# Performance work log

Measured on AMD Instinct MI355X. Metric: run time of the kernel, lower is better.

Reference implementation:

```python
import jax, jax.numpy as jnp
import numpy as np

B, D, NR, H = 8, 64, 6, 3        # batch, input_dim, num_relation, num_hop
R2 = 2 * NR                      # relations incl. inverses
NUM_RULE = R2 ** H               # 1728 combinatorial rules
EPS = 1e-6
TAU = 1.0


def _rule_indices():
    # torch.meshgrid (indexing='ij') over num_hop copies of arange(2*NR), stacked on last dim
    a = np.arange(R2)
    grids = np.meshgrid(*([a] * H), indexing="ij")
    return jnp.asarray(np.stack(grids, -1).reshape(-1, H))  # [NUM_RULE, H] int


def setup_inputs() -> dict:
    key = jax.random.key(0)
    ks = jax.random.split(key, 11)
    s = 0.1
    return {
        "query": jax.random.normal(ks[0], (B, D), jnp.float32),
        "relation_emb": jax.random.normal(ks[1], (R2, D), jnp.float32) * s,      # nn.Embedding(2*NR, D)
        "indicator": jax.random.normal(ks[2], (D,), jnp.float32) * s,            # nn.Embedding(1, D)
        "rel_W": jax.random.normal(ks[3], (H, D, R2 * D), jnp.float32) * s,      # per-layer relation_linear
        "rel_b": jax.random.normal(ks[4], (H, R2 * D), jnp.float32) * s,
        "lin_W": jax.random.normal(ks[5], (H, 13 * D, D), jnp.float32) * s,      # per-layer combine Linear(13D->D)
        "lin_b": jax.random.normal(ks[6], (H, D), jnp.float32) * s,
        "mlp_W1": jax.random.normal(ks[7], (2 * D, D), jnp.float32) * s,
        "mlp_b1": jax.random.normal(ks[8], (D,), jnp.float32) * s,
        "mlp_W2": jax.random.normal(ks[9], (D, 1), jnp.float32) * s,
        "mlp_b2": jax.random.normal(ks[10], (1,), jnp.float32) * s,
    }


def reference(query, relation_emb, indicator, rel_W, rel_b, lin_W, lin_b,
              mlp_W1, mlp_b1, mlp_W2, mlp_b2):
    rel_idx = _rule_indices()                       # [R, H]
    Rn = rel_idx.shape[0]

    # PNA degree scales: each graph is a chain; degree_out+1 (boundary self-message)
    # node 0 -> 1 message (boundary only), nodes 1..H -> 2 messages (edge + boundary)
    log_deg_head = jnp.log(jnp.float32(1.0))
    log_deg_tail = jnp.log(jnp.float32(2.0))
    mean_scale = (log_deg_head + H * log_deg_tail) / (H + 1)
    s_head = log_deg_head / mean_scale
    s_tail = log_deg_tail / mean_scale
    scales_head = jnp.stack([jnp.float32(1.0), s_head, 1.0 / jnp.maximum(s_head, 1e-2)])
    scales_tail = jnp.stack([jnp.float32(1.0), s_tail, 1.0 / jnp.maximum(s_tail, 1e-2)])

    # node-0 PNA update: single message == boundary == indicator (constant across graphs)
    # stats layout per feature dim: (mean, max, min, std)
    f0 = jnp.stack([indicator, indicator, indicator,
                    jnp.full((D,), float(np.sqrt(EPS)), indicator.dtype)], -1).reshape(4 * D)
    upd0 = (f0[:, None] * scales_head).reshape(12 * D)

    # boundary / initial hidden: indicator at node 0 of every graph
    hidden = jnp.zeros((B, Rn, H + 1, D), query.dtype)
    hidden = hidden.at[:, :, 0, :].set(indicator)

    for l in range(H):
        # dependent relation table from the query (relation_linear)
        rel_table = (query @ rel_W[l] + rel_b[l]).reshape(B, R2, D)
        rel = rel_table[:, rel_idx]                 # [B, R, H, D] gather per edge
        msg = hidden[:, :, :-1, :] * rel            # distmult message on edges h -> h+1
        # tail-node PNA stats over message set {msg, boundary=0}
        mean = msg * 0.5
        mx = jnp.maximum(msg, 0.0)
        mn = jnp.minimum(msg, 0.0)
        std = jnp.sqrt(jnp.maximum(msg * msg * 0.25, EPS))   # sq_mean - mean^2 = msg^2/4
        feats = jnp.stack([mean, mx, mn, std], -1).reshape(B, Rn, H, 4 * D)
        upd_tail = (feats[..., None] * scales_tail).reshape(B, Rn, H, 12 * D)
        upd = jnp.concatenate(
            [jnp.broadcast_to(upd0, (B, Rn, 1, 12 * D)), upd_tail], axis=2)
        # combine: relu(Linear(cat([input, update])))
        hidden = jax.nn.relu(
            jnp.concatenate([hidden, upd], -1) @ lin_W[l] + lin_b[l])

    # readout at tail node H, concat per-node query
    feat = jnp.concatenate(
        [hidden[:, :, H, :], jnp.broadcast_to(query[:, None, :], (B, Rn, D))], -1)
    score = (jax.nn.relu(feat @ mlp_W1 + mlp_b1) @ mlp_W2 + mlp_b2)[..., 0]   # [B, R]
    attention = jax.nn.softmax(score / TAU, axis=-1)
    r_emb = relation_emb[rel_idx]                   # [R, H, D]
    subgoals = jnp.einsum("br,rhd->bhd", attention, r_emb)
    masks = jnp.ones((B, H), bool)
    return subgoals, masks
```

## Files before the change

kernel.cpp:

```cpp
#include <hip/hip_runtime.h>
#include <hip/hip_bf16.h>


typedef const float* fp;

#define WS_WT     0
#define WS_RELT   49152
#define WS_QW1    67584
#define WS_Q2     68096
#define WS_QW3    141824
#define WS_SCORES 142592

__device__ __forceinline__ void accq(float4 mv, float4 tv,
                                     float4 wa, float4 wb, float4 wc, float4 wd,
                                     float& acc){
  acc += mv.x*wa.x; acc += fabsf(mv.x)*wa.y; acc += tv.x*wa.z;
  acc += mv.y*wb.x; acc += fabsf(mv.y)*wb.y; acc += tv.y*wb.z;
  acc += mv.z*wc.x; acc += fabsf(mv.z)*wc.y; acc += tv.z*wc.z;
  acc += mv.w*wd.x; acc += fabsf(mv.w)*wd.y; acc += tv.w*wd.z;
}

__global__ __launch_bounds__(256) void k_pre1(fp lin_W, fp query, fp rel_W,
                       fp rel_b, fp mlp_W1, fp mlp_b1, float* ws){
  __shared__ float sW[3072];
  __shared__ float part[4][64];
  int bi = blockIdx.x, tid = threadIdx.x;

  if (bi < 48){
    int l = bi>>4, d0 = (bi&15)*4;
    fp src = lin_W + (size_t)l*832*64 + (size_t)(64 + 12*d0)*64;
    float4* s4 = (float4*)sW;
    const float4* g4 = (const float4*)src;
    s4[tid] = g4[tid]; s4[tid+256] = g4[tid+256]; s4[tid+512] = g4[tid+512];
    __syncthreads();
    int c = tid&3, j = tid>>2;
    #pragma unroll
    for (int dd=0; dd<4; dd++){
      const float* W = sW + dd*768 + j;
      float v = 0.f;
      if (c == 0){
        float w0 = W[0]   + (4.f/3.f)*W[64]  + 0.75f*W[128];
        float w1 = W[192] + (4.f/3.f)*W[256] + 0.75f*W[320];
        float w2 = W[384] + (4.f/3.f)*W[448] + 0.75f*W[512];
        v = 0.5f*w0 + 0.5f*(w1 + w2);
      } else if (c == 1){
        float w1 = W[192] + (4.f/3.f)*W[256] + 0.75f*W[320];
        float w2 = W[384] + (4.f/3.f)*W[448] + 0.75f*W[512];
        v = 0.5f*(w1 - w2);
      } else if (c == 2){
        v = 0.5f*(W[576] + (4.f/3.f)*W[640] + 0.75f*W[704]);
      }
      ws[WS_WT + l*16384 + (d0+dd)*256 + tid] = v;
    }
  } else if (bi < 336){
    int idx = bi - 48;
    int l = idx/96; int rem = idx%96; int b = rem/12; int jj = rem%12;
    int d = tid&63, kc = tid>>6;
    fp W = rel_W + (size_t)l*64*768 + (size_t)(kc*16)*768 + jj*64 + d;
    fp q = query + b*64 + kc*16;
    float acc = (kc == 0) ? rel_b[l*768 + jj*64 + d] : 0.f;
    #pragma unroll
    for (int k=0;k<16;k++) acc += q[k] * W[k*768];
    part[kc][d] = acc;
    __syncthreads();
    if (tid < 64){
      float v = ((part[0][tid] + part[1][tid]) + part[2][tid]) + part[3][tid];
      ws[WS_RELT + l*6144 + b*768 + jj*64 + tid] = v;
    }
  } else {
    int b = bi - 336;
    int j = tid&63, kc = tid>>6;
    float acc = (kc == 0) ? mlp_b1[j] : 0.f;
    fp q = query + b*64 + kc*16;
    #pragma unroll
    for (int i=0;i<16;i++) acc += q[i] * mlp_W1[(64 + kc*16 + i)*64 + j];
    part[kc][j] = acc;
    __syncthreads();
    if (tid < 64){
      float v = ((part[0][tid] + part[1][tid]) + part[2][tid]) + part[3][tid];
      ws[WS_QW1 + b*64 + tid] = v;
    }
  }
}

__global__ void k_mid(fp indicator, fp lin_W, fp lin_b, float* ws){
  __shared__ float sC2[64], sC2W[64], sP1[64], sQ3[12][64];
  __shared__ __align__(16) float mP[64], tP[64];
  __shared__ __align__(16) float mL[12][64], tL[12][64];
  int tid = threadIdx.x;
  int w = tid>>6, j = tid&63;
  bool isQ2 = blockIdx.x < 96;
  int b  = isQ2 ? blockIdx.x/12 : blockIdx.x-96;
  int i0 = isQ2 ? blockIdx.x%12 : 0;
  if (w == 0){
    float acc = lin_b[j];
    #pragma unroll 8
    for (int d=0; d<64; d++) acc += 2e-3f * ws[WS_WT + ((d<<6)+j)*4 + 2];
    sC2[j] = fmaxf(acc, 0.f);
  } else if (w == 1 && isQ2){
    const float* rel = ws + WS_RELT + (b*12+i0)*64;
    float m = indicator[j] * rel[j];
    mP[j] = m; tP[j] = fmaxf(fabsf(m), 2e-3f);
  }
  __syncthreads();
  if (w == 0){
    float a2 = lin_b[64+j];
    fp W1 = lin_W + 832*64;
    #pragma unroll 16
    for (int k=0;k<64;k++) a2 += sC2[k] * W1[k*64+j];
    sC2W[j] = a2;
  } else if (w == 1 && isQ2){
    const float4* W4 = (const float4*)(ws + WS_WT);
    float acc = lin_b[j];
    #pragma unroll
    for (int dq=0; dq<16; dq++){
      float4 mv = ((const float4*)mP)[dq], tv = ((const float4*)tP)[dq];
      float4 wa = W4[(dq*4+0)*64+j], wb = W4[(dq*4+1)*64+j],
             wc = W4[(dq*4+2)*64+j], wd = W4[(dq*4+3)*64+j];
      accq(mv,tv,wa,wb,wc,wd,acc);
    }
    sP1[j] = fmaxf(acc, 0.f);
  }
  __syncthreads();
  {
    const float* rel = ws + WS_RELT + 6144 + (b*12+w)*64;
    float s = isQ2 ? sP1[j] : sC2[j];
    float m = s * rel[j];
    mL[w][j] = m; tL[w][j] = fmaxf(fabsf(m), 2e-3f);
  }
  __syncthreads();
  const float4* W4 = (const float4*)(ws + WS_WT + 16384);
  float acc = sC2W[j];
  #pragma unroll
  for (int dq=0; dq<16; dq++){
    float4 mv = ((const float4*)mL[w])[dq], tv = ((const float4*)tL[w])[dq];
    float4 wa = W4[(dq*4+0)*64+j], wb = W4[(dq*4+1)*64+j],
           wc = W4[(dq*4+2)*64+j], wd = W4[(dq*4+3)*64+j];
    accq(mv,tv,wa,wb,wc,wd,acc);
  }
  if (isQ2){
    ws[WS_Q2 + ((b*12+i0)*12+w)*64 + j] = fmaxf(acc, 0.f);
  } else {
    sQ3[w][j] = fmaxf(acc, 0.f);
    __syncthreads();
    fp W2 = lin_W + 2*832*64;
    float a = lin_b[128+j];
    #pragma unroll 16
    for (int k=0;k<64;k++) a += sQ3[w][k]*W2[k*64+j];
    ws[WS_QW3 + (b*12+w)*64 + j] = a;
  }
}

__global__ __launch_bounds__(256) void k_score(fp mlp_W1, fp mlp_W2, float* ws){
  __shared__ float wt_s[4096];
  __shared__ float fin[4][4][64];
  __shared__ __align__(16) float m_s[4][4][64];
  __shared__ __align__(16) float t_s[4][4][64];
  int tid = threadIdx.x, w = tid>>6, j = tid&63;
  int wave = blockIdx.x*4 + w;
  int b = blockIdx.x/108;
  int rem = wave%432;
  int i0 = rem/36; int t36 = rem%36;
  int i2 = t36/3;  int i1b = (t36%3)*4;
  {
    float rl = ws[WS_RELT + 12288 + (b*12+i2)*64 + j];
    #pragma unroll
    for (int r=0;r<4;r++){
      float qv = ws[WS_Q2 + ((b*12+i0)*12 + i1b + r)*64 + j];
      float m = qv*rl;
      m_s[w][r][j] = m;
      t_s[w][r][j] = fmaxf(fabsf(m), 2e-3f);
    }
  }
  float a0 = ws[WS_QW3 + (b*12+i2)*64 + j];
  float acc[4] = {a0, a0, a0, a0};
  const float4* Wt2 = (const float4*)(ws + WS_WT + 32768);
  for (int ch=0; ch<4; ch++){
    __syncthreads();
    {
      const float4* src = Wt2 + ch*1024;
      float4* dst = (float4*)wt_s;
      #pragma unroll
      for (int k=0; k<4; k++) dst[tid + k*256] = src[tid + k*256];
    }
    __syncthreads();
    #pragma unroll
    for (int dq=0; dq<4; dq++){
      int dc = ch*4 + dq;
      const float4* wl = (const float4*)wt_s + dq*256 + j;
      float4 wa = wl[0], wb = wl[64], wc = wl[128], wd = wl[192];
      #pragma unroll
      for (int r=0;r<4;r++){
        float4 mv = ((const float4*)m_s[w][r])[dc];
        float4 tv = ((const float4*)t_s[w][r])[dc];
        accq(mv,tv,wa,wb,wc,wd,acc[r]);
      }
    }
  }
  __syncthreads();
  fin[w][0][j]=fmaxf(acc[0],0.f); fin[w][1][j]=fmaxf(acc[1],0.f);
  fin[w][2][j]=fmaxf(acc[2],0.f); fin[w][3][j]=fmaxf(acc[3],0.f);
  __syncthreads();
  float qw = ws[WS_QW1 + b*64 + j];
  float w2v = mlp_W2[j];
  float h0=qw, h1=qw, h2=qw, h3=qw;
  #pragma unroll 8
  for (int i=0;i<64;i++){
    float wv = mlp_W1[i*64+j];
    h0 += fin[w][0][i]*wv; h1 += fin[w][1][i]*wv;
    h2 += fin[w][2][i]*wv; h3 += fin[w][3][i]*wv;
  }
  float s0=fmaxf(h0,0.f)*w2v, s1=fmaxf(h1,0.f)*w2v;
  float s2=fmaxf(h2,0.f)*w2v, s3=fmaxf(h3,0.f)*w2v;
  #pragma unroll
  for (int off=32; off>0; off>>=1){
    s0 += __shfl_down(s0, off, 64); s1 += __shfl_down(s1, off, 64);
    s2 += __shfl_down(s2, off, 64); s3 += __shfl_down(s3, off, 64);
  }
  if (j == 0){
    int rbase = i0*144 + i1b*12 + i2;
    float* S = ws + WS_SCORES + b*1728 + rbase;
    S[0] = s0; S[12] = s1; S[24] = s2; S[36] = s3;
  }
}

__global__ void k_final(fp relation_emb, float* ws, float* out){
  int b = blockIdx.x, tid = threadIdx.x;
  int w = tid>>6, lane = tid&63;
  __shared__ float se[1728];
  __shared__ float wred[4];
  __shared__ float pb[36][4];
  __shared__ float bins[36];
  const float* sc = ws + WS_SCORES + b*1728;
  float mx = -1e30f;
  for (int r=tid; r<1728; r+=256){ float v = sc[r]; se[r] = v; mx = fmaxf(mx, v); }
  #pragma unroll
  for (int off=32; off>0; off>>=1) mx = fmaxf(mx, __shfl_xor(mx, off, 64));
  if (lane == 0) wred[w] = mx;
  __syncthreads();
  mx = fmaxf(fmaxf(wred[0],wred[1]), fmaxf(wred[2],wred[3]));
  __syncthreads();
  float ts = 0.f;
  for (int r=tid; r<1728; r+=256){ float e = __expf(se[r]-mx); se[r] = e; ts += e; }
  #pragma unroll
  for (int off=32; off>0; off>>=1) ts += __shfl_xor(ts, off, 64);
  if (lane == 0) wred[w] = ts;
  __syncthreads();
  float tot = (wred[0]+wred[1]) + (wred[2]+wred[3]);
  if (tid < 144){
    int bin = tid>>2, q = tid&3;
    int h = bin/12, jj = bin%12;
    float a = 0.f;
    if (h == 0){
      const float* p = se + jj*144 + q*36;
      #pragma unroll 4
      for (int k=0;k<36;k++) a += p[k];
    } else if (h == 1){
      for (int t=q*36; t<q*36+36; t++) a += se[(t/12)*144 + jj*12 + (t%12)];
    } else {
      for (int t=q*36; t<q*36+36; t++) a += se[(t/12)*144 + (t%12)*12 + jj];
    }
    pb[bin][q] = a;
  }
  __syncthreads();
  if (tid < 36) bins[tid] = (pb[tid][0]+pb[tid][1]) + (pb[tid][2]+pb[tid][3]);
  __syncthreads();
  if (tid < 192){
    int h = tid>>6, d = tid&63;
    float acc = 0.f;
    #pragma unroll
    for (int jj=0; jj<12; jj++) acc += bins[h*12+jj] * relation_emb[jj*64+d];
    out[b*192 + tid] = acc/tot;
  }
  if (tid >= 192 && tid < 195){
    out[1536 + b*3 + (tid-192)] = 1.0f;
  }
}

extern "C" void kernel_launch(void* const* d_in, const int* in_sizes, int n_in,
                              void* d_out, int out_size, void* d_ws, size_t ws_size,
                              hipStream_t stream){
  fp query        = (fp)d_in[0];
  fp relation_emb = (fp)d_in[1];
  fp indicator    = (fp)d_in[2];
  fp rel_W        = (fp)d_in[3];
  fp rel_b        = (fp)d_in[4];
  fp lin_W        = (fp)d_in[5];
  fp lin_b        = (fp)d_in[6];
  fp mlp_W1       = (fp)d_in[7];
  fp mlp_b1       = (fp)d_in[8];
  fp mlp_W2       = (fp)d_in[9];
  float* ws = (float*)d_ws;
  float* out = (float*)d_out;

  k_pre1 <<<344, 256, 0, stream>>>(lin_W, query, rel_W, rel_b, mlp_W1, mlp_b1, ws);
  k_mid  <<<104, 768, 0, stream>>>(indicator, lin_W, lin_b, ws);
  k_score<<<864, 256, 0, stream>>>(mlp_W1, mlp_W2, ws);
  k_final<<<8,   256, 0, stream>>>(relation_emb, ws, out);
}
```

Before: 114.7 us.

## Move layer-2 precompute into k_mid and recompute clamped abs in-register

Work that only layer 2 and the readout need (layer-2 weight folding, layer-2 relation projection, query MLP term) moves out of k_pre1 into extra blocks of k_mid, so it runs alongside the mid-stage compute and k_pre1 gets shorter. Separately, the stored clamped-abs array t is dropped and fmaxf(fabsf(m), 2e-3) is recomputed inside accq. This cuts shared-memory footprint and LDS reads in k_score in exchange for a few extra ALU ops per element. The idle threads in the 768-thread helper blocks waste some occupancy.

```diff
diff --git a/kernel.cpp b/kernel.cpp
--- a/kernel.cpp
+++ b/kernel.cpp
@@ -11,22 +11,22 @@
 #define WS_QW3    141824
 #define WS_SCORES 142592
 
-__device__ __forceinline__ void accq(float4 mv, float4 tv,
+__device__ __forceinline__ void accq(float4 mv,
                                      float4 wa, float4 wb, float4 wc, float4 wd,
                                      float& acc){
-  acc += mv.x*wa.x; acc += fabsf(mv.x)*wa.y; acc += tv.x*wa.z;
-  acc += mv.y*wb.x; acc += fabsf(mv.y)*wb.y; acc += tv.y*wb.z;
-  acc += mv.z*wc.x; acc += fabsf(mv.z)*wc.y; acc += tv.z*wc.z;
-  acc += mv.w*wd.x; acc += fabsf(mv.w)*wd.y; acc += tv.w*wd.z;
+  acc += mv.x*wa.x; acc += fabsf(mv.x)*wa.y; acc += fmaxf(fabsf(mv.x),2e-3f)*wa.z;
+  acc += mv.y*wb.x; acc += fabsf(mv.y)*wb.y; acc += fmaxf(fabsf(mv.y),2e-3f)*wb.z;
+  acc += mv.z*wc.x; acc += fabsf(mv.z)*wc.y; acc += fmaxf(fabsf(mv.z),2e-3f)*wc.z;
+  acc += mv.w*wd.x; acc += fabsf(mv.w)*wd.y; acc += fmaxf(fabsf(mv.w),2e-3f)*wd.z;
 }
 
 __global__ __launch_bounds__(256) void k_pre1(fp lin_W, fp query, fp rel_W,
-                       fp rel_b, fp mlp_W1, fp mlp_b1, float* ws){
+                       fp rel_b, float* ws){
   __shared__ float sW[3072];
   __shared__ float part[4][64];
   int bi = blockIdx.x, tid = threadIdx.x;
 
-  if (bi < 48){
+  if (bi < 32){
     int l = bi>>4, d0 = (bi&15)*4;
     fp src = lin_W + (size_t)l*832*64 + (size_t)(64 + 12*d0)*64;
     float4* s4 = (float4*)sW;
@@ -52,8 +52,8 @@
       }
       ws[WS_WT + l*16384 + (d0+dd)*256 + tid] = v;
     }
-  } else if (bi < 336){
-    int idx = bi - 48;
+  } else {
+    int idx = bi - 32;
     int l = idx/96; int rem = idx%96; int b = rem/12; int jj = rem%12;
     int d = tid&63, kc = tid>>6;
     fp W = rel_W + (size_t)l*64*768 + (size_t)(kc*16)*768 + jj*64 + d;
@@ -67,31 +67,89 @@
       float v = ((part[0][tid] + part[1][tid]) + part[2][tid]) + part[3][tid];
       ws[WS_RELT + l*6144 + b*768 + jj*64 + tid] = v;
     }
-  } else {
-    int b = bi - 336;
-    int j = tid&63, kc = tid>>6;
-    float acc = (kc == 0) ? mlp_b1[j] : 0.f;
-    fp q = query + b*64 + kc*16;
-    #pragma unroll
-    for (int i=0;i<16;i++) acc += q[i] * mlp_W1[(64 + kc*16 + i)*64 + j];
-    part[kc][j] = acc;
-    __syncthreads();
-    if (tid < 64){
-      float v = ((part[0][tid] + part[1][tid]) + part[2][tid]) + part[3][tid];
-      ws[WS_QW1 + b*64 + tid] = v;
-    }
-  }
-}
-
-__global__ void k_mid(fp indicator, fp lin_W, fp lin_b, float* ws){
+  }
+}
+
+__global__ __launch_bounds__(768) void k_mid(fp indicator, fp lin_W, fp lin_b,
+                       fp query, fp rel_W, fp rel_b, fp mlp_W1, fp mlp_b1,
+                       float* ws){
   __shared__ float sC2[64], sC2W[64], sP1[64], sQ3[12][64];
-  __shared__ __align__(16) float mP[64], tP[64];
-  __shared__ __align__(16) float mL[12][64], tL[12][64];
-  int tid = threadIdx.x;
+  __shared__ __align__(16) float mP[64];
+  __shared__ __align__(16) float mL[12][64];
+  __shared__ float sW[3072];
+  __shared__ float part[4][64];
+  int bi = blockIdx.x, tid = threadIdx.x;
+
+  if (bi >= 104){
+    if (bi < 120){
+      int d0 = (bi-104)*4;
+      if (tid < 256){
+        fp src = lin_W + (size_t)2*832*64 + (size_t)(64 + 12*d0)*64;
+        float4* s4 = (float4*)sW;
+        const float4* g4 = (const float4*)src;
+        s4[tid] = g4[tid]; s4[tid+256] = g4[tid+256]; s4[tid+512] = g4[tid+512];
+      }
+      __syncthreads();
+      if (tid < 256){
+        int c = tid&3, j = tid>>2;
+        #pragma unroll
+        for (int dd=0; dd<4; dd++){
+          const float* W = sW + dd*768 + j;
+          float v = 0.f;
+          if (c == 0){
+            float w0 = W[0]   + (4.f/3.f)*W[64]  + 0.75f*W[128];
+            float w1 = W[192] + (4.f/3.f)*W[256] + 0.75f*W[320];
+            float w2 = W[384] + (4.f/3.f)*W[448] + 0.75f*W[512];
+            v = 0.5f*w0 + 0.5f*(w1 + w2);
+          } else if (c == 1){
+            float w1 = W[192] + (4.f/3.f)*W[256] + 0.75f*W[320];
+            float w2 = W[384] + (4.f/3.f)*W[448] + 0.75f*W[512];
+            v = 0.5f*(w1 - w2);
+          } else if (c == 2){
+            v = 0.5f*(W[576] + (4.f/3.f)*W[640] + 0.75f*W[704]);
+          }
+          ws[WS_WT + 2*16384 + (d0+dd)*256 + tid] = v;
+        }
+      }
+    } else if (bi < 216){
+      int idx = bi - 120; int b = idx/12; int jj = idx%12;
+      if (tid < 256){
+        int d = tid&63, kc = tid>>6;
+        fp W = rel_W + (size_t)2*64*768 + (size_t)(kc*16)*768 + jj*64 + d;
+        fp q = query + b*64 + kc*16;
+        float acc = (kc == 0) ? rel_b[2*768 + jj*64 + d] : 0.f;
+        #pragma unroll
+        for (int k=0;k<16;k++) acc += q[k] * W[k*768];
+        part[kc][d] = acc;
+      }
+      __syncthreads();
+      if (tid < 64){
+        float v = ((part[0][tid] + part[1][tid]) + part[2][tid]) + part[3][tid];
+        ws[WS_RELT + 2*6144 + b*768 + jj*64 + tid] = v;
+      }
+    } else {
+      int b = bi - 216;
+      if (tid < 256){
+        int j = tid&63, kc = tid>>6;
+        float acc = (kc == 0) ? mlp_b1[j] : 0.f;
+        fp q = query + b*64 + kc*16;
+        #pragma unroll
+        for (int i=0;i<16;i++) acc += q[i] * mlp_W1[(64 + kc*16 + i)*64 + j];
+        part[kc][j] = acc;
+      }
+      __syncthreads();
+      if (tid < 64){
+        float v = ((part[0][tid] + part[1][tid]) + part[2][tid]) + part[3][tid];
+        ws[WS_QW1 + b*64 + tid] = v;
+      }
+    }
+    return;
+  }
+
   int w = tid>>6, j = tid&63;
-  bool isQ2 = blockIdx.x < 96;
-  int b  = isQ2 ? blockIdx.x/12 : blockIdx.x-96;
-  int i0 = isQ2 ? blockIdx.x%12 : 0;
+  bool isQ2 = bi < 96;
+  int b  = isQ2 ? bi/12 : bi-96;
+  int i0 = isQ2 ? bi%12 : 0;
   if (w == 0){
     float acc = lin_b[j];
     #pragma unroll 8
@@ -99,8 +157,7 @@
     sC2[j] = fmaxf(acc, 0.f);
   } else if (w == 1 && isQ2){
     const float* rel = ws + WS_RELT + (b*12+i0)*64;
-    float m = indicator[j] * rel[j];
-    mP[j] = m; tP[j] = fmaxf(fabsf(m), 2e-3f);
+    mP[j] = indicator[j] * rel[j];
   }
   __syncthreads();
   if (w == 0){
@@ -114,10 +171,10 @@
     float acc = lin_b[j];
     #pragma unroll
     for (int dq=0; dq<16; dq++){
-      float4 mv = ((const float4*)mP)[dq], tv = ((const float4*)tP)[dq];
+      float4 mv = ((const float4*)mP)[dq];
       float4 wa = W4[(dq*4+0)*64+j], wb = W4[(dq*4+1)*64+j],
              wc = W4[(dq*4+2)*64+j], wd = W4[(dq*4+3)*64+j];
-      accq(mv,tv,wa,wb,wc,wd,acc);
+      accq(mv,wa,wb,wc,wd,acc);
     }
     sP1[j] = fmaxf(acc, 0.f);
   }
@@ -125,18 +182,17 @@
   {
     const float* rel = ws + WS_RELT + 6144 + (b*12+w)*64;
     float s = isQ2 ? sP1[j] : sC2[j];
-    float m = s * rel[j];
-    mL[w][j] = m; tL[w][j] = fmaxf(fabsf(m), 2e-3f);
+    mL[w][j] = s * rel[j];
   }
   __syncthreads();
   const float4* W4 = (const float4*)(ws + WS_WT + 16384);
   float acc = sC2W[j];
   #pragma unroll
   for (int dq=0; dq<16; dq++){
-    float4 mv = ((const float4*)mL[w])[dq], tv = ((const float4*)tL[w])[dq];
+    float4 mv = ((const float4*)mL[w])[dq];
     float4 wa = W4[(dq*4+0)*64+j], wb = W4[(dq*4+1)*64+j],
            wc = W4[(dq*4+2)*64+j], wd = W4[(dq*4+3)*64+j];
-    accq(mv,tv,wa,wb,wc,wd,acc);
+    accq(mv,wa,wb,wc,wd,acc);
   }
   if (isQ2){
     ws[WS_Q2 + ((b*12+i0)*12+w)*64 + j] = fmaxf(acc, 0.f);
@@ -155,7 +211,6 @@
   __shared__ float wt_s[4096];
   __shared__ float fin[4][4][64];
   __shared__ __align__(16) float m_s[4][4][64];
-  __shared__ __align__(16) float t_s[4][4][64];
   int tid = threadIdx.x, w = tid>>6, j = tid&63;
   int wave = blockIdx.x*4 + w;
   int b = blockIdx.x/108;
@@ -167,9 +222,7 @@
     #pragma unroll
     for (int r=0;r<4;r++){
       float qv = ws[WS_Q2 + ((b*12+i0)*12 + i1b + r)*64 + j];
-      float m = qv*rl;
-      m_s[w][r][j] = m;
-      t_s[w][r][j] = fmaxf(fabsf(m), 2e-3f);
+      m_s[w][r][j] = qv*rl;
     }
   }
   float a0 = ws[WS_QW3 + (b*12+i2)*64 + j];
@@ -192,8 +245,7 @@
       #pragma unroll
       for (int r=0;r<4;r++){
         float4 mv = ((const float4*)m_s[w][r])[dc];
-        float4 tv = ((const float4*)t_s[w][r])[dc];
-        accq(mv,tv,wa,wb,wc,wd,acc[r]);
+        accq(mv,wa,wb,wc,wd,acc[r]);
       }
     }
   }
@@ -293,8 +345,9 @@
   float* ws = (float*)d_ws;
   float* out = (float*)d_out;
 
-  k_pre1 <<<344, 256, 0, stream>>>(lin_W, query, rel_W, rel_b, mlp_W1, mlp_b1, ws);
-  k_mid  <<<104, 768, 0, stream>>>(indicator, lin_W, lin_b, ws);
+  k_pre1 <<<224, 256, 0, stream>>>(lin_W, query, rel_W, rel_b, ws);
+  k_mid  <<<224, 768, 0, stream>>>(indicator, lin_W, lin_b, query, rel_W, rel_b,
+                                   mlp_W1, mlp_b1, ws);
   k_score<<<864, 256, 0, stream>>>(mlp_W1, mlp_W2, ws);
   k_final<<<8,   256, 0, stream>>>(relation_emb, ws, out);
 }
```

After: 115.4 us. No clear change (+0.6%).
